# Kernel optimization log

Hardware: AMD Instinct MI355X
Metric: run time of the kernel (lower is better)

## Reference

```python
import jax, jax.numpy as jnp
import numpy as np
import math

N, T, NS, NO, HID = 256, 1000, 10, 10, 64


def gru_seq(x, Wi, Wh, bi, bh):
    # x: [N,T,D] -> hidden states [N,T,HID] (single-layer GRU, h0 = 0)
    xproj = x @ Wi + bi  # [N,T,3H], precompute input projections
    def step(h, xp):
        hp = h @ Wh + bh
        xr, xz, xn = jnp.split(xp, 3, axis=-1)
        hr, hz, hn = jnp.split(hp, 3, axis=-1)
        r = jax.nn.sigmoid(xr + hr)
        z = jax.nn.sigmoid(xz + hz)
        n = jnp.tanh(xn + r * hn)
        h_new = (1.0 - z) * n + z * h
        return h_new, h_new
    h0 = jnp.zeros((x.shape[0], Wh.shape[0]), x.dtype)
    _, hs = jax.lax.scan(step, h0, jnp.swapaxes(xproj, 0, 1))
    return jnp.swapaxes(hs, 0, 1)


def setup_inputs() -> dict:
    key = jax.random.key(0)
    ks = jax.random.split(key, 12)
    D = NO + NS  # GRU input = concat(y, x_hat)
    s = lambda fan: 1.0 / np.sqrt(fan)
    inp = {
        "Yi_batch": jax.random.normal(ks[0], (N, T, NO), jnp.float32),
        "X_hat_batch": jax.random.normal(ks[1], (N, T, NS), jnp.float32),
        # per-sample observation noise covariance: 0.5*I plus small random diagonal
        "Cw_batch": 0.5 * jnp.eye(NO, dtype=jnp.float32)[None] + jnp.eye(NO)[None] * 0.1 * jax.random.uniform(ks[2], (N, 1, 1), jnp.float32),
        "H": jax.random.normal(ks[3], (NO, NS), jnp.float32) * s(NS),
        "mu_w": jnp.zeros((NO, 1), jnp.float32),
        "Wi": jax.random.normal(ks[4], (D, 3 * HID), jnp.float32) * s(D),
        "Wh": jax.random.normal(ks[5], (HID, 3 * HID), jnp.float32) * s(HID),
        "bi": jnp.zeros((3 * HID,), jnp.float32),
        "bh": jnp.zeros((3 * HID,), jnp.float32),
        "W_mu": jax.random.normal(ks[6], (HID, NS), jnp.float32) * s(HID),
        "b_mu": jnp.zeros((NS,), jnp.float32),
        "W_var": jax.random.normal(ks[7], (HID, NS), jnp.float32) * s(HID),
        "b_var": jnp.zeros((NS,), jnp.float32),
    }
    return inp


def reference(Yi_batch, X_hat_batch, Cw_batch, H, mu_w, Wi, Wh, bi, bh, W_mu, b_mu, W_var, b_var):
    n_obs = Yi_batch.shape[-1]
    Tlen = Yi_batch.shape[1]
    # RNN: mu and (positive) vars per time step
    hs = gru_seq(jnp.concatenate([Yi_batch, X_hat_batch], axis=-1), Wi, Wh, bi, bh)
    mu_prev = hs @ W_mu + b_mu                       # [N,T,NS]
    var_prev = jax.nn.softplus(hs @ W_var + b_var)   # [N,T,NS] diag of L_xt_yt_prev
    # marginal over y: mu_y = H mu_prev + mu_w ; L_y = H diag(var) H^T + Cw
    mu_y = jnp.einsum('ij,ntj->nti', H, mu_prev) + mu_w[:, 0]
    HLH = jnp.einsum('ij,ntj,kj->ntik', H, var_prev, H)   # [N,T,NO,NO]
    L_y = HLH + Cw_batch[:, None]                          # broadcast Cw over time
    e = Yi_batch - mu_y
    # Gaussian log-likelihood via Cholesky (L_y is SPD)
    chol = jnp.linalg.cholesky(L_y)
    logdet = 2.0 * jnp.sum(jnp.log(jnp.diagonal(chol, axis1=-2, axis2=-1)), axis=-1)  # [N,T]
    sol = jnp.linalg.solve(L_y, e[..., None])[..., 0]
    quad = jnp.sum(e * sol, axis=-1)                       # [N,T]
    logprob = (-0.5 * n_obs * Tlen * math.log(2.0 * math.pi)
               - 0.5 * jnp.sum(logdet, axis=1)
               - 0.5 * jnp.sum(quad, axis=1))              # [N]
    return jnp.mean(logprob / (Tlen * n_obs))
```

## Files before the change

### kernel.cpp

```cpp
#include <hip/hip_runtime.h>
#include <math.h>

#define BN 256
#define TT 1000
#define NO 10
#define NS 10
#define HID 64
#define DIN 20
#define G3 192
#define SPB 16
#define NB (BN / SPB)
#define GS 8
#define NG 125
#define C_HALF_LOG2PI -0.918938533204672742f

typedef _Float16 f16x8 __attribute__((ext_vector_type(8)));
typedef float f32x4 __attribute__((ext_vector_type(4)));

__device__ __forceinline__ float rcpf(float x) { return __builtin_amdgcn_rcpf(x); }

__device__ __forceinline__ void sync_lds() {
    asm volatile("s_waitcnt lgkmcnt(0)\n\ts_barrier" ::: "memory");
}

__device__ __forceinline__ f32x4 mfma16(f16x8 a, f16x8 b, f32x4 c) {
    return __builtin_amdgcn_mfma_f32_16x16x32_f16(a, b, c, 0, 0, 0);
}

__global__ __attribute__((amdgpu_flat_work_group_size(256, 256)))
void gru_mfma(const float* __restrict__ Yi, const float* __restrict__ Xh,
              const float* __restrict__ Wi, const float* __restrict__ Wh,
              const float* __restrict__ bi, const float* __restrict__ bh,
              const float* __restrict__ Wmu, const float* __restrict__ Wvar,
              float* __restrict__ mv_out) {
    const int tid = threadIdx.x;
    const int lane = tid & 63;
    const int w = tid >> 6;
    const int c = lane & 15;
    const int q = lane >> 4;

    __shared__ _Float16 hbuf[2][SPB][72];
    __shared__ _Float16 xbuf[2][GS][SPB][40];

    const int base = blockIdx.x * SPB;

    {
        int* p = (int*)&hbuf[0][0][0];
        for (int i = tid; i < (int)(sizeof(hbuf) / 4); i += 256) p[i] = 0;
        int* p2 = (int*)&xbuf[0][0][0][0];
        for (int i = tid; i < (int)(sizeof(xbuf) / 4); i += 256) p2[i] = 0;
    }
    sync_lds();

    const int col_g = 16 * w + c;
    f16x8 fWr0, fWr1, fWz0, fWz1, fWn0, fWn1;
    f16x8 fIr, fIz, fIn;
    f16x8 fM0, fM1;
#pragma unroll
    for (int j = 0; j < 8; ++j) {
        const int k0 = 8 * q + j;
        const int k1 = 32 + 8 * q + j;
        fWr0[j] = (_Float16)Wh[k0 * G3 + col_g];
        fWr1[j] = (_Float16)Wh[k1 * G3 + col_g];
        fWz0[j] = (_Float16)Wh[k0 * G3 + 64 + col_g];
        fWz1[j] = (_Float16)Wh[k1 * G3 + 64 + col_g];
        fWn0[j] = (_Float16)Wh[k0 * G3 + 128 + col_g];
        fWn1[j] = (_Float16)Wh[k1 * G3 + 128 + col_g];
        fIr[j] = (k0 < DIN) ? (_Float16)Wi[k0 * G3 + col_g] : (_Float16)0.0f;
        fIz[j] = (k0 < DIN) ? (_Float16)Wi[k0 * G3 + 64 + col_g] : (_Float16)0.0f;
        fIn[j] = (k0 < DIN) ? (_Float16)Wi[k0 * G3 + 128 + col_g] : (_Float16)0.0f;
        float m0 = 0.0f, m1 = 0.0f;
        const int d = 16 * w + c;
        if (w < 2 && d < DIN) {
            m0 = (d < NS) ? Wmu[k0 * NS + d] : Wvar[k0 * NS + (d - NS)];
            m1 = (d < NS) ? Wmu[k1 * NS + d] : Wvar[k1 * NS + (d - NS)];
        }
        fM0[j] = (_Float16)m0;
        fM1[j] = (_Float16)m1;
    }
    const int u = col_g;
    const float b_r = bi[u] + bh[u];
    const float b_z = bi[64 + u] + bh[64 + u];
    const float bxn = bi[128 + u];
    const float bhn = bh[128 + u];

    const int sty = (tid < 128) ? tid : tid - 128;
    const int ss = sty >> 4;
    const int sm = sty & 15;
    const float* srow = (tid < 128) ? (Yi + (size_t)(base + sm) * TT * NO)
                                    : (Xh + (size_t)(base + sm) * TT * NS);
    const int k0s = (tid < 128) ? 0 : 10;

    {
        const float* rp = srow + (size_t)ss * 10;
#pragma unroll
        for (int e = 0; e < 10; ++e)
            xbuf[0][ss][sm][k0s + e] = (_Float16)rp[e];
    }
    sync_lds();

    float hprev[4] = {0.0f, 0.0f, 0.0f, 0.0f};

#pragma unroll 1
    for (int g = 0; g < NG; ++g) {
        float st[10];
        const bool do_ld = (g + 1 < NG);
        if (do_ld) {
            const float* rp = srow + (size_t)(8 * (g + 1) + ss) * 10;
#pragma unroll
            for (int e = 0; e < 10; ++e) st[e] = rp[e];
        }
#pragma unroll
        for (int s = 0; s < GS; ++s) {
            const int t = 8 * g + s;
            const int p = t & 1;
            const f16x8 ha0 = *(const f16x8*)&hbuf[p][c][8 * q];
            const f16x8 ha1 = *(const f16x8*)&hbuf[p][c][32 + 8 * q];
            const f16x8 xa  = *(const f16x8*)&xbuf[g & 1][s][c][8 * q];
            f32x4 Dr = {0, 0, 0, 0}, Dz = {0, 0, 0, 0};
            f32x4 Dnx = {0, 0, 0, 0}, Dnh = {0, 0, 0, 0};
            Dr  = mfma16(xa, fIr, Dr);
            Dz  = mfma16(xa, fIz, Dz);
            Dnx = mfma16(xa, fIn, Dnx);
            Dr  = mfma16(ha0, fWr0, Dr);
            Dz  = mfma16(ha0, fWz0, Dz);
            Dnh = mfma16(ha0, fWn0, Dnh);
            Dr  = mfma16(ha1, fWr1, Dr);
            Dz  = mfma16(ha1, fWz1, Dz);
            Dnh = mfma16(ha1, fWn1, Dnh);
            f32x4 Dmv = {0, 0, 0, 0};
            if (w < 2) {
                Dmv = mfma16(ha0, fM0, Dmv);
                Dmv = mfma16(ha1, fM1, Dmv);
            }
#pragma unroll
            for (int j = 0; j < 4; ++j) {
                const float ar = Dr[j] + b_r;
                const float az = Dz[j] + b_z;
                const float ax = Dnx[j] + bxn;
                const float ah = Dnh[j] + bhn;
                const float r = rcpf(1.0f + __expf(-ar));
                const float z = rcpf(1.0f + __expf(-az));
                const float pre = fmaf(r, ah, ax);
                const float e2 = __expf(2.0f * pre);
                const float nn = 1.0f - 2.0f * rcpf(e2 + 1.0f);
                const float hn = fmaf(z, hprev[j] - nn, nn);
                hprev[j] = hn;
                hbuf[p ^ 1][4 * q + j][u] = (_Float16)hn;
            }
            if (t > 0 && w < 2) {
                const int d0 = 16 * w + c;
                if (d0 < DIN) {
#pragma unroll
                    for (int j = 0; j < 4; ++j) {
                        const size_t row = (size_t)(base + 4 * q + j) * TT + (t - 1);
                        mv_out[row * DIN + d0] = Dmv[j];
                    }
                }
            }
            if (s == GS - 1 && do_ld) {
#pragma unroll
                for (int e = 0; e < 10; ++e)
                    xbuf[(g + 1) & 1][ss][sm][k0s + e] = (_Float16)st[e];
            }
            sync_lds();
        }
    }

    if (w < 2) {
        const f16x8 ha0 = *(const f16x8*)&hbuf[0][c][8 * q];
        const f16x8 ha1 = *(const f16x8*)&hbuf[0][c][32 + 8 * q];
        f32x4 Dmv = {0, 0, 0, 0};
        Dmv = mfma16(ha0, fM0, Dmv);
        Dmv = mfma16(ha1, fM1, Dmv);
        const int d0 = 16 * w + c;
        if (d0 < DIN) {
#pragma unroll
            for (int j = 0; j < 4; ++j) {
                const size_t row = (size_t)(base + 4 * q + j) * TT + (TT - 1);
                mv_out[row * DIN + d0] = Dmv[j];
            }
        }
    }
}

__global__ __launch_bounds__(256)
void lik_p2(const float* __restrict__ Yi, const float* __restrict__ Cw,
            const float* __restrict__ Hm, const float* __restrict__ mu_w,
            const float* __restrict__ b_mu, const float* __restrict__ b_var,
            const float* __restrict__ mv_in, float* __restrict__ out) {
    __shared__ float sH[NO * NS];
    __shared__ float smw[NO], sbm[NS], sbv[NS];
    __shared__ float ssum[4];
    const int tid = threadIdx.x;
    if (tid < NO * NS) sH[tid] = Hm[tid];
    if (tid < NO) smw[tid] = mu_w[tid];
    if (tid < NS) { sbm[tid] = b_mu[tid]; sbv[tid] = b_var[tid]; }
    __syncthreads();

    const int gid = blockIdx.x * 256 + tid;
    float contrib = 0.0f;
    if (gid < BN * TT) {
        const int n = gid / TT;
        const float* mv = mv_in + (size_t)gid * DIN;
        float mu[NS], va[NS];
#pragma unroll
        for (int i = 0; i < NS; ++i) {
            mu[i] = mv[i] + sbm[i];
            float x = mv[NS + i] + sbv[i];
            va[i] = (x > 0.0f) ? (x + log1pf(__expf(-x))) : log1pf(__expf(x));
        }
        const float* y = Yi + (size_t)gid * NO;
        float e[NO];
#pragma unroll
        for (int i = 0; i < NO; ++i) {
            float m = smw[i];
#pragma unroll
            for (int j = 0; j < NS; ++j) m = fmaf(sH[i * NS + j], mu[j], m);
            e[i] = y[i] - m;
        }
        float M[NO][NO];
        const float* cw = Cw + (size_t)n * NO * NO;
#pragma unroll
        for (int i = 0; i < NO; ++i)
#pragma unroll
            for (int j = 0; j <= i; ++j) M[i][j] = cw[i * NO + j];
#pragma unroll
        for (int l = 0; l < NS; ++l) {
            float vl = va[l];
            float hv[NO];
#pragma unroll
            for (int i = 0; i < NO; ++i) hv[i] = sH[i * NS + l];
#pragma unroll
            for (int i = 0; i < NO; ++i) {
                float hvi = hv[i] * vl;
#pragma unroll
                for (int j = 0; j <= i; ++j) M[i][j] = fmaf(hvi, hv[j], M[i][j]);
            }
        }
        float dprod = 1.0f;
        float drs[NO];
#pragma unroll
        for (int j = 0; j < NO; ++j) {
            float d = M[j][j];
#pragma unroll
            for (int k = 0; k < j; ++k) d = fmaf(-M[j][k], M[j][k], d);
            dprod *= d;
            float rs = __frsqrt_rn(d);
            drs[j] = rs;
#pragma unroll
            for (int i = j + 1; i < NO; ++i) {
                float v = M[i][j];
#pragma unroll
                for (int k = 0; k < j; ++k) v = fmaf(-M[i][k], M[j][k], v);
                M[i][j] = v * rs;
            }
        }
        const float logdet = __logf(dprod);
        float wv[NO];
        float quad = 0.0f;
#pragma unroll
        for (int i = 0; i < NO; ++i) {
            float v = e[i];
#pragma unroll
            for (int k = 0; k < i; ++k) v = fmaf(-M[i][k], wv[k], v);
            wv[i] = v * drs[i];
            quad = fmaf(wv[i], wv[i], quad);
        }
        const float SCALE = 0.5f / ((float)BN * (float)TT * (float)NO);
        contrib = -(logdet + quad) * SCALE;
    }

#pragma unroll
    for (int off = 32; off > 0; off >>= 1) contrib += __shfl_down(contrib, off);
    if ((tid & 63) == 0) ssum[tid >> 6] = contrib;
    __syncthreads();
    if (tid == 0) {
        float s = ssum[0] + ssum[1] + ssum[2] + ssum[3];
        if (blockIdx.x == 0) s += C_HALF_LOG2PI;
        atomicAdd(out, s);
    }
}

extern "C" void kernel_launch(void* const* d_in, const int* in_sizes, int n_in,
                              void* d_out, int out_size, void* d_ws, size_t ws_size,
                              hipStream_t stream) {
    const float* Yi    = (const float*)d_in[0];
    const float* Xh    = (const float*)d_in[1];
    const float* Cw    = (const float*)d_in[2];
    const float* Hm    = (const float*)d_in[3];
    const float* mu_w  = (const float*)d_in[4];
    const float* Wi    = (const float*)d_in[5];
    const float* Wh    = (const float*)d_in[6];
    const float* bi    = (const float*)d_in[7];
    const float* bh    = (const float*)d_in[8];
    const float* W_mu  = (const float*)d_in[9];
    const float* b_mu  = (const float*)d_in[10];
    const float* W_var = (const float*)d_in[11];
    const float* b_var = (const float*)d_in[12];
    float* out = (float*)d_out;
    float* mv  = (float*)d_ws;

    hipMemsetAsync(d_out, 0, sizeof(float), stream);
    gru_mfma<<<dim3(NB), dim3(256), 0, stream>>>(Yi, Xh, Wi, Wh, bi, bh,
                                                 W_mu, W_var, mv);
    lik_p2<<<dim3((BN * TT + 255) / 256), dim3(256), 0, stream>>>(
        Yi, Cw, Hm, mu_w, b_mu, b_var, mv, out);
}
```

Before: 603.4 us.

## Halve samples per GRU block to 8 and use two-wave blocks

The recurrent GRU kernel now processes 8 sequences per block with 128 threads (2 waves) instead of 16 sequences with 4 waves. Each wave computes two 16-column hidden-unit tiles, and MFMA rows 8-15 are padding. The grid doubles from 16 to 32 blocks, so more CUs share the serial 1000-step recurrence. The cost is twice as many MFMAs per wave and wasted MFMA rows, which lengthens the per-step critical path.

```diff
diff --git a/kernel.cpp b/kernel.cpp
--- a/kernel.cpp
+++ b/kernel.cpp
@@ -8,8 +8,8 @@
 #define HID 64
 #define DIN 20
 #define G3 192
-#define SPB 16
-#define NB (BN / SPB)
+#define SPB 8
+#define NBLK (BN / SPB)
 #define GS 8
 #define NG 125
 #define C_HALF_LOG2PI -0.918938533204672742f
@@ -27,69 +27,78 @@
     return __builtin_amdgcn_mfma_f32_16x16x32_f16(a, b, c, 0, 0, 0);
 }
 
-__global__ __attribute__((amdgpu_flat_work_group_size(256, 256)))
-void gru_mfma(const float* __restrict__ Yi, const float* __restrict__ Xh,
-              const float* __restrict__ Wi, const float* __restrict__ Wh,
-              const float* __restrict__ bi, const float* __restrict__ bh,
-              const float* __restrict__ Wmu, const float* __restrict__ Wvar,
-              float* __restrict__ mv_out) {
+__global__ __attribute__((amdgpu_flat_work_group_size(128, 128)))
+void gru_mfma2(const float* __restrict__ Yi, const float* __restrict__ Xh,
+               const float* __restrict__ Wi, const float* __restrict__ Wh,
+               const float* __restrict__ bi, const float* __restrict__ bh,
+               const float* __restrict__ Wmu, const float* __restrict__ Wvar,
+               float* __restrict__ mv_out) {
     const int tid = threadIdx.x;
     const int lane = tid & 63;
     const int w = tid >> 6;
     const int c = lane & 15;
     const int q = lane >> 4;
 
-    __shared__ _Float16 hbuf[2][SPB][72];
-    __shared__ _Float16 xbuf[2][GS][SPB][40];
+    __shared__ _Float16 hbuf[2][16][72];
+    __shared__ _Float16 xbuf[2][GS][16][40];
 
     const int base = blockIdx.x * SPB;
 
     {
         int* p = (int*)&hbuf[0][0][0];
-        for (int i = tid; i < (int)(sizeof(hbuf) / 4); i += 256) p[i] = 0;
+        for (int i = tid; i < (int)(sizeof(hbuf) / 4); i += 128) p[i] = 0;
         int* p2 = (int*)&xbuf[0][0][0][0];
-        for (int i = tid; i < (int)(sizeof(xbuf) / 4); i += 256) p2[i] = 0;
+        for (int i = tid; i < (int)(sizeof(xbuf) / 4); i += 128) p2[i] = 0;
     }
     sync_lds();
 
-    const int col_g = 16 * w + c;
-    f16x8 fWr0, fWr1, fWz0, fWz1, fWn0, fWn1;
-    f16x8 fIr, fIz, fIn;
+    const int uA = 32 * w + c;
+    const int uB = 32 * w + 16 + c;
+    f16x8 Ar0, Ar1, Az0, Az1, An0, An1, AIr, AIz, AIn;
+    f16x8 Br0, Br1, Bz0, Bz1, Bn0, Bn1, BIr, BIz, BIn;
     f16x8 fM0, fM1;
+    const int dmv = 16 * w + c;
+    const bool mv_ok = (dmv < DIN);
 #pragma unroll
     for (int j = 0; j < 8; ++j) {
         const int k0 = 8 * q + j;
         const int k1 = 32 + 8 * q + j;
-        fWr0[j] = (_Float16)Wh[k0 * G3 + col_g];
-        fWr1[j] = (_Float16)Wh[k1 * G3 + col_g];
-        fWz0[j] = (_Float16)Wh[k0 * G3 + 64 + col_g];
-        fWz1[j] = (_Float16)Wh[k1 * G3 + 64 + col_g];
-        fWn0[j] = (_Float16)Wh[k0 * G3 + 128 + col_g];
-        fWn1[j] = (_Float16)Wh[k1 * G3 + 128 + col_g];
-        fIr[j] = (k0 < DIN) ? (_Float16)Wi[k0 * G3 + col_g] : (_Float16)0.0f;
-        fIz[j] = (k0 < DIN) ? (_Float16)Wi[k0 * G3 + 64 + col_g] : (_Float16)0.0f;
-        fIn[j] = (k0 < DIN) ? (_Float16)Wi[k0 * G3 + 128 + col_g] : (_Float16)0.0f;
+        Ar0[j] = (_Float16)Wh[k0 * G3 + uA];
+        Ar1[j] = (_Float16)Wh[k1 * G3 + uA];
+        Az0[j] = (_Float16)Wh[k0 * G3 + 64 + uA];
+        Az1[j] = (_Float16)Wh[k1 * G3 + 64 + uA];
+        An0[j] = (_Float16)Wh[k0 * G3 + 128 + uA];
+        An1[j] = (_Float16)Wh[k1 * G3 + 128 + uA];
+        Br0[j] = (_Float16)Wh[k0 * G3 + uB];
+        Br1[j] = (_Float16)Wh[k1 * G3 + uB];
+        Bz0[j] = (_Float16)Wh[k0 * G3 + 64 + uB];
+        Bz1[j] = (_Float16)Wh[k1 * G3 + 64 + uB];
+        Bn0[j] = (_Float16)Wh[k0 * G3 + 128 + uB];
+        Bn1[j] = (_Float16)Wh[k1 * G3 + 128 + uB];
+        AIr[j] = (k0 < DIN) ? (_Float16)Wi[k0 * G3 + uA] : (_Float16)0.0f;
+        AIz[j] = (k0 < DIN) ? (_Float16)Wi[k0 * G3 + 64 + uA] : (_Float16)0.0f;
+        AIn[j] = (k0 < DIN) ? (_Float16)Wi[k0 * G3 + 128 + uA] : (_Float16)0.0f;
+        BIr[j] = (k0 < DIN) ? (_Float16)Wi[k0 * G3 + uB] : (_Float16)0.0f;
+        BIz[j] = (k0 < DIN) ? (_Float16)Wi[k0 * G3 + 64 + uB] : (_Float16)0.0f;
+        BIn[j] = (k0 < DIN) ? (_Float16)Wi[k0 * G3 + 128 + uB] : (_Float16)0.0f;
         float m0 = 0.0f, m1 = 0.0f;
-        const int d = 16 * w + c;
-        if (w < 2 && d < DIN) {
-            m0 = (d < NS) ? Wmu[k0 * NS + d] : Wvar[k0 * NS + (d - NS)];
-            m1 = (d < NS) ? Wmu[k1 * NS + d] : Wvar[k1 * NS + (d - NS)];
+        if (mv_ok) {
+            m0 = (dmv < NS) ? Wmu[k0 * NS + dmv] : Wvar[k0 * NS + (dmv - NS)];
+            m1 = (dmv < NS) ? Wmu[k1 * NS + dmv] : Wvar[k1 * NS + (dmv - NS)];
         }
         fM0[j] = (_Float16)m0;
         fM1[j] = (_Float16)m1;
     }
-    const int u = col_g;
-    const float b_r = bi[u] + bh[u];
-    const float b_z = bi[64 + u] + bh[64 + u];
-    const float bxn = bi[128 + u];
-    const float bhn = bh[128 + u];
-
-    const int sty = (tid < 128) ? tid : tid - 128;
-    const int ss = sty >> 4;
-    const int sm = sty & 15;
-    const float* srow = (tid < 128) ? (Yi + (size_t)(base + sm) * TT * NO)
-                                    : (Xh + (size_t)(base + sm) * TT * NS);
-    const int k0s = (tid < 128) ? 0 : 10;
+    const float brA = bi[uA] + bh[uA], brB = bi[uB] + bh[uB];
+    const float bzA = bi[64 + uA] + bh[64 + uA], bzB = bi[64 + uB] + bh[64 + uB];
+    const float bxA = bi[128 + uA], bxB = bi[128 + uB];
+    const float bhA = bh[128 + uA], bhB = bh[128 + uB];
+
+    const int sm = tid & 7;
+    const int ss = (tid >> 3) & 7;
+    const float* srow = (tid < 64) ? (Yi + (size_t)(base + sm) * TT * NO)
+                                   : (Xh + (size_t)(base + sm) * TT * NS);
+    const int k0s = (tid < 64) ? 0 : 10;
 
     {
         const float* rp = srow + (size_t)ss * 10;
@@ -99,7 +108,8 @@
     }
     sync_lds();
 
-    float hprev[4] = {0.0f, 0.0f, 0.0f, 0.0f};
+    float hpA[4] = {0, 0, 0, 0};
+    float hpB[4] = {0, 0, 0, 0};
 
 #pragma unroll 1
     for (int g = 0; g < NG; ++g) {
@@ -117,45 +127,65 @@
             const f16x8 ha0 = *(const f16x8*)&hbuf[p][c][8 * q];
             const f16x8 ha1 = *(const f16x8*)&hbuf[p][c][32 + 8 * q];
             const f16x8 xa  = *(const f16x8*)&xbuf[g & 1][s][c][8 * q];
-            f32x4 Dr = {0, 0, 0, 0}, Dz = {0, 0, 0, 0};
-            f32x4 Dnx = {0, 0, 0, 0}, Dnh = {0, 0, 0, 0};
-            Dr  = mfma16(xa, fIr, Dr);
-            Dz  = mfma16(xa, fIz, Dz);
-            Dnx = mfma16(xa, fIn, Dnx);
-            Dr  = mfma16(ha0, fWr0, Dr);
-            Dz  = mfma16(ha0, fWz0, Dz);
-            Dnh = mfma16(ha0, fWn0, Dnh);
-            Dr  = mfma16(ha1, fWr1, Dr);
-            Dz  = mfma16(ha1, fWz1, Dz);
-            Dnh = mfma16(ha1, fWn1, Dnh);
             f32x4 Dmv = {0, 0, 0, 0};
-            if (w < 2) {
-                Dmv = mfma16(ha0, fM0, Dmv);
-                Dmv = mfma16(ha1, fM1, Dmv);
-            }
+            Dmv = mfma16(ha0, fM0, Dmv);
+            Dmv = mfma16(ha1, fM1, Dmv);
+            if (t > 0 && mv_ok && q < 2) {
+#pragma unroll
+                for (int j = 0; j < 4; ++j) {
+                    const size_t row = (size_t)(base + 4 * q + j) * TT + (t - 1);
+                    mv_out[row * DIN + dmv] = Dmv[j];
+                }
+            }
+            f32x4 DrA = {0,0,0,0}, DzA = {0,0,0,0}, DxA = {0,0,0,0}, DhA = {0,0,0,0};
+            DrA = mfma16(xa, AIr, DrA);
+            DzA = mfma16(xa, AIz, DzA);
+            DxA = mfma16(xa, AIn, DxA);
+            DrA = mfma16(ha0, Ar0, DrA);
+            DzA = mfma16(ha0, Az0, DzA);
+            DhA = mfma16(ha0, An0, DhA);
+            DrA = mfma16(ha1, Ar1, DrA);
+            DzA = mfma16(ha1, Az1, DzA);
+            DhA = mfma16(ha1, An1, DhA);
+            f32x4 DrB = {0,0,0,0}, DzB = {0,0,0,0}, DxB = {0,0,0,0}, DhB = {0,0,0,0};
+            DrB = mfma16(xa, BIr, DrB);
+            DzB = mfma16(xa, BIz, DzB);
+            DxB = mfma16(xa, BIn, DxB);
+            DrB = mfma16(ha0, Br0, DrB);
+            DzB = mfma16(ha0, Bz0, DzB);
+            DhB = mfma16(ha0, Bn0, DhB);
+            DrB = mfma16(ha1, Br1, DrB);
+            DzB = mfma16(ha1, Bz1, DzB);
+            DhB = mfma16(ha1, Bn1, DhB);
 #pragma unroll
             for (int j = 0; j < 4; ++j) {
-                const float ar = Dr[j] + b_r;
-                const float az = Dz[j] + b_z;
-                const float ax = Dnx[j] + bxn;
-                const float ah = Dnh[j] + bhn;
-                const float r = rcpf(1.0f + __expf(-ar));
-                const float z = rcpf(1.0f + __expf(-az));
-                const float pre = fmaf(r, ah, ax);
-                const float e2 = __expf(2.0f * pre);
-                const float nn = 1.0f - 2.0f * rcpf(e2 + 1.0f);
-                const float hn = fmaf(z, hprev[j] - nn, nn);
-                hprev[j] = hn;
-                hbuf[p ^ 1][4 * q + j][u] = (_Float16)hn;
-            }
-            if (t > 0 && w < 2) {
-                const int d0 = 16 * w + c;
-                if (d0 < DIN) {
-#pragma unroll
-                    for (int j = 0; j < 4; ++j) {
-                        const size_t row = (size_t)(base + 4 * q + j) * TT + (t - 1);
-                        mv_out[row * DIN + d0] = Dmv[j];
-                    }
+                {
+                    const float ar = DrA[j] + brA;
+                    const float az = DzA[j] + bzA;
+                    const float ax = DxA[j] + bxA;
+                    const float ah = DhA[j] + bhA;
+                    const float r = rcpf(1.0f + __expf(-ar));
+                    const float z = rcpf(1.0f + __expf(-az));
+                    const float pre = fmaf(r, ah, ax);
+                    const float e2 = __expf(2.0f * pre);
+                    const float nn = 1.0f - 2.0f * rcpf(e2 + 1.0f);
+                    const float hn = fmaf(z, hpA[j] - nn, nn);
+                    hpA[j] = hn;
+                    if (q < 2) hbuf[p ^ 1][4 * q + j][uA] = (_Float16)hn;
+                }
+                {
+                    const float ar = DrB[j] + brB;
+                    const float az = DzB[j] + bzB;
+                    const float ax = DxB[j] + bxB;
+                    const float ah = DhB[j] + bhB;
+                    const float r = rcpf(1.0f + __expf(-ar));
+                    const float z = rcpf(1.0f + __expf(-az));
+                    const float pre = fmaf(r, ah, ax);
+                    const float e2 = __expf(2.0f * pre);
+                    const float nn = 1.0f - 2.0f * rcpf(e2 + 1.0f);
+                    const float hn = fmaf(z, hpB[j] - nn, nn);
+                    hpB[j] = hn;
+                    if (q < 2) hbuf[p ^ 1][4 * q + j][uB] = (_Float16)hn;
                 }
             }
             if (s == GS - 1 && do_ld) {
@@ -167,18 +197,17 @@
         }
     }
 
-    if (w < 2) {
+    {
         const f16x8 ha0 = *(const f16x8*)&hbuf[0][c][8 * q];
         const f16x8 ha1 = *(const f16x8*)&hbuf[0][c][32 + 8 * q];
         f32x4 Dmv = {0, 0, 0, 0};
         Dmv = mfma16(ha0, fM0, Dmv);
         Dmv = mfma16(ha1, fM1, Dmv);
-        const int d0 = 16 * w + c;
-        if (d0 < DIN) {
+        if (mv_ok && q < 2) {
 #pragma unroll
             for (int j = 0; j < 4; ++j) {
                 const size_t row = (size_t)(base + 4 * q + j) * TT + (TT - 1);
-                mv_out[row * DIN + d0] = Dmv[j];
+                mv_out[row * DIN + dmv] = Dmv[j];
             }
         }
     }
@@ -302,8 +331,8 @@
     float* mv  = (float*)d_ws;
 
     hipMemsetAsync(d_out, 0, sizeof(float), stream);
-    gru_mfma<<<dim3(NB), dim3(256), 0, stream>>>(Yi, Xh, Wi, Wh, bi, bh,
-                                                 W_mu, W_var, mv);
+    gru_mfma2<<<dim3(NBLK), dim3(128), 0, stream>>>(Yi, Xh, Wi, Wh, bi, bh,
+                                                    W_mu, W_var, mv);
     lik_p2<<<dim3((BN * TT + 255) / 256), dim3(256), 0, stream>>>(
         Yi, Cw, Hm, mu_w, b_mu, b_var, mv, out);
 }
```

After: 932.3 us. +54.5%, slower.
